# Performance work log

Hardware: AMD Instinct MI355X
Metric: run time of the kernel (lower is better)

The kernel has to match this reference:

```python
import jax, jax.numpy as jnp
import numpy as np

H = 4          # attention heads
K = 16         # knn neighbors
EPS = 1e-5     # BatchNorm eps


def setup_inputs() -> dict:
    key = jax.random.key(0)
    ks = jax.random.split(key, 10)
    B, C, T, N = 2, 128, 32, 512
    OUT = 128
    HID = 2 * C + 2 * OUT  # ff hidden = in*2 + out*2
    s = 0.02
    return {
        "x_all": jax.random.normal(ks[0], (B, C, T, N), jnp.float32),
        "Wq": jax.random.normal(ks[1], (C, C), jnp.float32) * s,
        "Wk": jax.random.normal(ks[2], (C, C), jnp.float32) * s,
        "Wv": jax.random.normal(ks[3], (C, C), jnp.float32) * s,
        "W1": jax.random.normal(ks[4], (HID, C), jnp.float32) * s,
        "W2": jax.random.normal(ks[5], (OUT, HID), jnp.float32) * s,
        "bn_gamma": 1.0 + 0.1 * jax.random.normal(ks[6], (OUT,), jnp.float32),
        "bn_beta": 0.1 * jax.random.normal(ks[7], (OUT,), jnp.float32),
        "bn_mean": 0.1 * jax.random.normal(ks[8], (OUT,), jnp.float32),
        "bn_var": jax.random.uniform(ks[9], (OUT,), jnp.float32, 0.5, 1.5),
    }


def reference(x_all, Wq, Wk, Wv, W1, W2, bn_gamma, bn_beta, bn_mean, bn_var):
    B, C, T, N = x_all.shape
    D = C // H
    # --- st_group_points: candidate pool = 3 consecutive frames (replicate temporal pad), frame-major ---
    xp = jnp.concatenate([x_all[:, :, :1], x_all, x_all[:, :, -1:]], axis=2)   # (B,C,T+2,N)
    pool = jnp.stack([xp[:, :, :-2], xp[:, :, 1:-1], xp[:, :, 2:]], axis=3)    # (B,C,T,3,N)
    pool = pool.reshape(B, C, T, 3 * N)                                        # (B,C,T,3N)
    # KNN on xyz (channels 0:3); sqrt is monotone so topk on squared dists gives same indices
    a = x_all[:, :3]                                                           # (B,3,T,N)
    b = pool[:, :3]                                                            # (B,3,T,3N)
    d2 = jnp.sum((a[..., :, None] - b[..., None, :]) ** 2, axis=1)             # (B,T,N,3N)
    _, idx = jax.lax.top_k(-d2, K)                                             # (B,T,N,K) smallest-dist
    nb = jnp.take_along_axis(pool[:, :, :, None, :], idx[:, None], axis=-1)    # (B,C,T,N,K)
    rel = x_all[..., None] - nb                                                # diff grouping (B,C,T,N,K)
    # --- per-point local attention over K neighbors (1x1 convs == channel matmuls), all t at once ---
    q = jnp.einsum('oc,bctn->botn', Wq, x_all).reshape(B, H, D, T, N)
    k = jnp.einsum('oc,bctnk->botnk', Wk, rel).reshape(B, H, D, T, N, K)
    v = jnp.einsum('oc,bctnk->botnk', Wv, rel).reshape(B, H, D, T, N, K)
    energy = jnp.einsum('bhdtn,bhdtnk->bhtnk', q, k) / jnp.sqrt(jnp.float32(D))
    attn = jax.nn.softmax(energy, axis=-1)                                     # (B,H,T,N,K)
    agg = jnp.einsum('bhtnk,bhdtnk->bhdtn', attn, v).reshape(B, C, T, N)
    # --- residual + BatchNorm1d (eval mode, running stats) + conv feed-forward ---
    h = x_all + agg
    scale = (bn_gamma / jnp.sqrt(bn_var + EPS))[None, :, None, None]
    h = (h - bn_mean[None, :, None, None]) * scale + bn_beta[None, :, None, None]
    h = jax.nn.leaky_relu(jnp.einsum('oc,bctn->botn', W1, h), 0.2)
    y = jnp.einsum('oc,bctn->botn', W2, h)                                     # (B,OUT,T,N)
    return jnp.concatenate([x_all[:, :4], y], axis=1)                          # (B,4+OUT,T,N)
```

## Files before the change

### kernel.cpp

```cpp
#include <hip/hip_runtime.h>
#include <hip/hip_bf16.h>

typedef __hip_bfloat16 bf16;
typedef unsigned long long u64;
typedef __attribute__((ext_vector_type(8))) short short8;
typedef __attribute__((ext_vector_type(4))) float f32x4;

#define B_   2
#define C_   128
#define T_   32
#define N_   512
#define K_   16
#define HID_ 512
#define TN   (T_*N_)
#define PTS  (B_*T_*N_)

#define MFMA_BF16(a,b,c) __builtin_amdgcn_mfma_f32_16x16x32_bf16((a),(b),(c),0,0,0)

__device__ __forceinline__ float b2f(bf16 v){ return __bfloat162float(v); }
__device__ __forceinline__ bf16  f2b(float v){ return __float2bfloat16(v); }
__device__ __forceinline__ float bqf(short v){
  return __uint_as_float(((unsigned)(unsigned short)v) << 16);
}

__device__ __forceinline__ float ldc(const void* p, int i, bool f32) {
  return f32 ? ((const float*)p)[i] : b2f(((const bf16*)p)[i]);
}

__global__ __launch_bounds__(256) void convw_kernel(
    const void* __restrict__ x,
    const void* wq, const void* wk, const void* wv,
    const void* w1, const void* w2, const void* g, const void* bb,
    const void* m, const void* v,
    bf16* __restrict__ wqb, bf16* __restrict__ wkb, bf16* __restrict__ wvb,
    bf16* __restrict__ w1b, bf16* __restrict__ w2b,
    float* __restrict__ gf, float* __restrict__ bf_, float* __restrict__ mf,
    float* __restrict__ vf, int* __restrict__ flag)
{
  __shared__ int cnt;
  if (threadIdx.x == 0) cnt = 0;
  __syncthreads();
  const unsigned short* u = (const unsigned short*)x;
  int w = 0;
#pragma unroll
  for (int j = 0; j < 8; ++j) {
    unsigned short hv = u[threadIdx.x*8 + j];
    int e = (hv >> 7) & 0xFF;
    if (e >= 0x89) w++;
  }
  if (w) atomicAdd(&cnt, w);
  __syncthreads();
  bool f32 = (cnt > 32);
  if (blockIdx.x == 0 && threadIdx.x == 0) *flag = f32 ? 1 : 0;

  int i = blockIdx.x*256 + threadIdx.x;
  if (i < 16384) { wqb[i] = f2b(ldc(wq, i, f32)); return; } i -= 16384;
  if (i < 16384) { wkb[i] = f2b(ldc(wk, i, f32)); return; } i -= 16384;
  if (i < 16384) { wvb[i] = f2b(ldc(wv, i, f32)); return; } i -= 16384;
  if (i < 65536) { w1b[i] = f2b(ldc(w1, i, f32)); return; } i -= 65536;
  if (i < 65536) { w2b[i] = f2b(ldc(w2, i, f32)); return; } i -= 65536;
  if (i < 128)   { gf[i]  = ldc(g, i, f32); return; }       i -= 128;
  if (i < 128)   { bf_[i] = ldc(bb, i, f32); return; }      i -= 128;
  if (i < 128)   { mf[i]  = ldc(m, i, f32); return; }       i -= 128;
  if (i < 128)   { vf[i]  = ldc(v, i, f32); return; }
}

__device__ __forceinline__ u64 shflx64(u64 v, int m) {
  return (u64)__shfl_xor((long long)v, m, 64);
}
template<int W>
__device__ __forceinline__ u64 bitonic64w(u64 key, int lane) {
#pragma unroll
  for (int k = 2; k <= W; k <<= 1) {
#pragma unroll
    for (int j = k >> 1; j >= 1; j >>= 1) {
      u64 p = shflx64(key, j);
      bool keep_min = ((lane & k) == 0) == ((lane & j) == 0);
      key = ((p < key) == keep_min) ? p : key;
    }
  }
  return key;
}
__device__ __forceinline__ unsigned bitonic32u(unsigned key, int lane) {
#pragma unroll
  for (int k = 2; k <= 64; k <<= 1) {
#pragma unroll
    for (int j = k >> 1; j >= 1; j >>= 1) {
      unsigned p = (unsigned)__shfl_xor((int)key, j, 64);
      bool keep_min = ((lane & k) == 0) == ((lane & j) == 0);
      key = ((p < key) == keep_min) ? p : key;
    }
  }
  return key;
}

__device__ __forceinline__ void proj_gemm32(const bf16* __restrict__ W,
                                            bf16 (*ys)[136],
                                            const short8 am[2][4],
                                            int mrow, int quad, int ot)
{
  f32x4 acc[2];
#pragma unroll
  for (int mt=0;mt<2;++mt) acc[mt] = (f32x4){0.f,0.f,0.f,0.f};
#pragma unroll
  for (int kq=0;kq<4;++kq) {
    short8 bfr = *(const short8*)&W[(ot*16+mrow)*C_ + kq*32 + quad*8];
#pragma unroll
    for (int mt=0;mt<2;++mt) acc[mt] = MFMA_BF16(am[mt][kq], bfr, acc[mt]);
  }
#pragma unroll
  for (int mt=0;mt<2;++mt)
#pragma unroll
    for (int r=0;r<4;++r)
      ys[mt*16 + quad*4 + r][ot*16 + mrow] = f2b(acc[mt][r]);
}

__device__ __forceinline__ void tile_store32_512(bf16* __restrict__ dst,
                                                 const bf16 (*ys)[136], int tid)
{
  int flat = tid*8;
  int p = flat >> 7, c = flat & 127;
  *(short8*)&dst[(size_t)p*C_ + c] = *(const short8*)&ys[p][c];
}

__global__ __launch_bounds__(512) void projknn_kernel(
    const void* __restrict__ x, const int* __restrict__ flag,
    const bf16* __restrict__ wqb, const bf16* __restrict__ wkb, const bf16* __restrict__ wvb,
    bf16* __restrict__ xTb, bf16* QT, bf16* __restrict__ KT, bf16* __restrict__ VT,
    int* __restrict__ idxout)
{
  __shared__ __align__(16) char smem[28672];
  int tid = threadIdx.x;
  int blk = blockIdx.x;
  int g = blk / 5, r = blk - g*5;
  if (r == 4) {
    bf16 (*xs )[136] = (bf16(*)[136])(smem);
    bf16 (*ysK)[136] = (bf16(*)[136])(smem + 8704);
    bf16 (*ysV)[136] = (bf16(*)[136])(smem + 17408);
    int p0 = g * 32;
    int b = p0 >> 14; int tn0 = p0 & (TN-1);
    if (*flag) {
      const float* xbase = (const float*)x + (size_t)b*C_*TN + tn0;
#pragma unroll
      for (int it=0; it<8; ++it) {
        int i = it*512 + tid;
        int c = i >> 5, p = i & 31;
        xs[p][c] = f2b(xbase[(size_t)c*TN + p]);
      }
    } else {
      const bf16* xbase = (const bf16*)x + (size_t)b*C_*TN + tn0;
#pragma unroll
      for (int it=0; it<8; ++it) {
        int i = it*512 + tid;
        int c = i >> 5, p = i & 31;
        xs[p][c] = xbase[(size_t)c*TN + p];
      }
    }
    __syncthreads();
    tile_store32_512(xTb + (size_t)p0*C_, xs, tid);
    int lane = tid & 63, wave = tid >> 6;
    int mrow = lane & 15, quad = lane >> 4;
    short8 am[2][4];
#pragma unroll
    for (int mt=0;mt<2;++mt)
#pragma unroll
      for (int kq=0;kq<4;++kq)
        am[mt][kq] = *(const short8*)&xs[mt*16 + mrow][kq*32 + quad*8];
    __syncthreads();
    proj_gemm32(wqb, xs,  am, mrow, quad, wave);
    proj_gemm32(wkb, ysK, am, mrow, quad, wave);
    proj_gemm32(wvb, ysV, am, mrow, quad, wave);
    __syncthreads();
    tile_store32_512(QT + (size_t)p0*C_, xs,  tid);
    tile_store32_512(KT + (size_t)p0*C_, ysK, tid);
    tile_store32_512(VT + (size_t)p0*C_, ysV, tid);
  } else {
    float4* cand4 = (float4*)smem;
    u64 (*surv)[64] = (u64(*)[64])(smem + 24576);
    int kblk = g*4 + r;
    int row = kblk >> 6;
    int b = row >> 5, t = row & 31;
    int ng = kblk & 63;
    bool f32 = (*flag != 0);
#pragma unroll
    for (int q = 0; q < 3; ++q) {
      int tt = t - 1 + q; tt = tt < 0 ? 0 : (tt > T_-1 ? T_-1 : tt);
      size_t base = ((size_t)b*C_*T_ + tt)*(size_t)N_ + tid;
      float c0, c1, c2;
      if (f32) {
        const float* xp = (const float*)x;
        c0 = xp[base]; c1 = xp[base + (size_t)T_*N_]; c2 = xp[base + 2*(size_t)T_*N_];
      } else {
        const bf16* xp = (const bf16*)x;
        c0 = b2f(xp[base]); c1 = b2f(xp[base + (size_t)T_*N_]); c2 = b2f(xp[base + 2*(size_t)T_*N_]);
      }
      cand4[q*N_ + tid] = make_float4(c0, c1, c2, 0.f);
    }
    __syncthreads();
    int wave = tid >> 6, lane = tid & 63;
    int n = ng*8 + wave;
    float4 a = cand4[N_ + n];
    unsigned db[24];
#pragma unroll
    for (int j = 0; j < 24; ++j) {
      float4 cm = cand4[lane + (j << 6)];
      float dx = a.x - cm.x;
      float dy = a.y - cm.y;
      float dz = a.z - cm.z;
      float d2 = __fadd_rn(__fadd_rn(__fmul_rn(dx,dx), __fmul_rn(dy,dy)), __fmul_rn(dz,dz));
      db[j] = __float_as_uint(d2);
    }
    unsigned bd = db[0];
#pragma unroll
    for (int j = 1; j < 24; ++j) bd = (db[j] < bd) ? db[j] : bd;
    unsigned sd = bitonic32u(bd, lane);
    unsigned U = (unsigned)__shfl((int)sd, 15, 64);
    int c = 0;
#pragma unroll
    for (int j = 0; j < 24; ++j) c += (db[j] <= U) ? 1 : 0;
    int sc = c;
#pragma unroll
    for (int d = 1; d < 64; d <<= 1) {
      int pv = __shfl_up(sc, d, 64);
      if (lane >= d) sc += pv;
    }
    int total = __shfl(sc, 63, 64);
    int ofs = sc - c;
    u64 out16;
    if (total <= 64) {
#pragma unroll
      for (int j = 0; j < 24; ++j) {
        if (db[j] <= U) {
          surv[wave][ofs] = ((u64)db[j] << 32) | (unsigned)(lane + (j << 6));
          ++ofs;
        }
      }
      __threadfence_block();
      u64 kk = (lane < total) ? surv[wave][lane] : ~0ull;
      out16 = (total <= 32) ? bitonic64w<32>(kk, lane)
                            : bitonic64w<64>(kk, lane);
    } else {
      u64 key[24];
#pragma unroll
      for (int j = 0; j < 24; ++j)
        key[j] = ((u64)db[j] << 32) | (unsigned)(lane + (j << 6));
      u64 res = ~0ull;
#pragma unroll 1
      for (int rr = 0; rr < 16; ++rr) {
        u64 m2 = key[0];
#pragma unroll
        for (int j = 1; j < 24; ++j) m2 = (key[j] < m2) ? key[j] : m2;
#pragma unroll
        for (int s = 32; s >= 1; s >>= 1) {
          u64 p = shflx64(m2, s);
          m2 = (p < m2) ? p : m2;
        }
        if (lane == rr) res = m2;
        int mwin = (int)(m2 & 0xffffffffu);
        int sel = ((mwin & 63) == lane) ? (mwin >> 6) : -1;
#pragma unroll
        for (int j = 0; j < 24; ++j) if (j == sel) key[j] = ~0ull;
      }
      out16 = res;
    }
    int point = (b*T_ + t)*N_ + n;
    if (lane < K_) idxout[point*K_ + lane] = (int)(out16 & 0xffffffffu);
  }
}

__global__ __launch_bounds__(512) void attn_kernel(
    const int* __restrict__ idxin, const bf16* __restrict__ xTb,
    bf16* qhT , const bf16* __restrict__ KT,
    const bf16* __restrict__ VT,
    const float* __restrict__ gf, const float* __restrict__ bf_,
    const float* __restrict__ mf, const float* __restrict__ vf)
{
  __shared__ int   col_lds[4][16];
  __shared__ float qbuf[4][C_];
  __shared__ bf16  kbuf[4][K_][136];
  __shared__ bf16  vbuf[4][K_][136];
  __shared__ float e_lds[4][4][16];
  int tid = threadIdx.x;
  int pt = tid >> 7, o = tid & 127;
  int point = blockIdx.x*4 + pt;
  int b = point >> 14; int tn = point & (TN-1); int t = tn >> 9;
  if (o < K_) {
    int m = idxin[point*K_ + o];
    int j = m >> 9, nn = m & (N_-1);
    int tt = t-1+j; tt = tt<0?0:(tt>T_-1?T_-1:tt);
    col_lds[pt][o] = ((b*T_ + tt)*N_ + nn)*C_;
  }
  int self = point*C_;
  qbuf[pt][o] = b2f(qhT[self + o]);
  __syncthreads();
#pragma unroll
  for (int it = 0; it < 2; ++it) {
    int i = it*512 + tid;
    int pp = i >> 8, rem = i & 255, k = rem >> 4, ch = rem & 15;
    int src = col_lds[pp][k] + ch*8;
    *(short8*)&kbuf[pp][k][ch*8] = *(const short8*)&KT[src];
    *(short8*)&vbuf[pp][k][ch*8] = *(const short8*)&VT[src];
  }
  __syncthreads();
  {
    int pp = tid >> 7, j = tid & 127;
    int k = j >> 3, hd = (j >> 1) & 3, half = j & 1;
    const float* qp = &qbuf[pp][hd*32 + half*16];
    const bf16*  kp = &kbuf[pp][k][hd*32 + half*16];
    short8 kv0 = *(const short8*)kp;
    short8 kv1 = *(const short8*)(kp + 8);
    float qv[16];
    *(float4*)&qv[0]  = *(const float4*)(qp);
    *(float4*)&qv[4]  = *(const float4*)(qp + 4);
    *(float4*)&qv[8]  = *(const float4*)(qp + 8);
    *(float4*)&qv[12] = *(const float4*)(qp + 12);
    float e = 0.f;
#pragma unroll
    for (int i2=0;i2<8;++i2) e = fmaf(qv[i2],   bqf(kv0[i2]), e);
#pragma unroll
    for (int i2=0;i2<8;++i2) e = fmaf(qv[8+i2], bqf(kv1[i2]), e);
    e += __shfl_xor(e, 1, 64);
    if (!half) e_lds[pp][hd][k] = -e * 0.17677669529663687f;
  }
  __syncthreads();
  int hd = o >> 5;
  float e[16]; float mx = -3e38f;
#pragma unroll
  for (int k=0;k<K_;++k){ e[k]=e_lds[pt][hd][k]; mx=fmaxf(mx,e[k]); }
  float ssum=0.f;
#pragma unroll
  for (int k=0;k<K_;++k){ e[k]=__expf(e[k]-mx); ssum+=e[k]; }
  float inv = 1.f/ssum;
  float acc = b2f(VT[self + o]);
#pragma unroll
  for (int k=0;k<K_;++k)
    acc = fmaf(-(e[k]*inv), b2f(vbuf[pt][k][o]), acc);
  float hv = b2f(xTb[self + o]) + acc;
  float sc = gf[o] / sqrtf(vf[o] + 1e-5f);
  qhT[self + o] = f2b((hv - mf[o])*sc + bf_[o]);
}

__global__ __launch_bounds__(256) void mlp_kernel(const bf16* __restrict__ hT,
                                                  const bf16* __restrict__ w1b,
                                                  const bf16* __restrict__ w2b,
                                                  const void* __restrict__ x,
                                                  const int* __restrict__ flag,
                                                  void* out)
{
  __shared__ bf16 hidh[32][264];
  int tid = threadIdx.x;
  int p0 = blockIdx.x*32;
  int lane = tid & 63, wave = tid >> 6;
  int mrow = lane & 15, quad = lane >> 4;
  bool f32o = (*flag != 0);
  int bb = p0 >> 14;
  int tn0 = p0 & (TN-1);
  if (tid < 128) {
    int c = tid >> 5, p = tid & 31;
    size_t si = ((size_t)bb*C_ + c)*TN + tn0 + p;
    size_t di = ((size_t)bb*132 + c)*TN + tn0 + p;
    if (f32o) ((float*)out)[di] = ((const float*)x)[si];
    else      ((bf16*)out)[di]  = ((const bf16*)x)[si];
  }
  f32x4 acc2[2][2];
#pragma unroll
  for (int oi=0;oi<2;++oi)
#pragma unroll
    for (int mt=0;mt<2;++mt) acc2[oi][mt] = (f32x4){0.f,0.f,0.f,0.f};

#pragma unroll
  for (int half = 0; half < 2; ++half) {
    if (half) __syncthreads();
    short8 am[2][4];
#pragma unroll
    for (int mt=0;mt<2;++mt)
#pragma unroll
      for (int kq=0;kq<4;++kq)
        am[mt][kq] = *(const short8*)&hT[(size_t)(p0 + mt*16 + mrow)*C_ + kq*32 + quad*8];
#pragma unroll
    for (int oi = 0; oi < 4; ++oi) {
      int ot_g = half*16 + wave*4 + oi;
      int otl  = wave*4 + oi;
      f32x4 acc[2];
#pragma unroll
      for (int mt=0;mt<2;++mt) acc[mt] = (f32x4){0.f,0.f,0.f,0.f};
#pragma unroll
      for (int kq=0;kq<4;++kq) {
        short8 bfr = *(const short8*)&w1b[(ot_g*16+mrow)*C_ + kq*32 + quad*8];
#pragma unroll
        for (int mt=0;mt<2;++mt) acc[mt] = MFMA_BF16(am[mt][kq], bfr, acc[mt]);
      }
#pragma unroll
      for (int mt=0;mt<2;++mt)
#pragma unroll
        for (int r=0;r<4;++r) {
          float z = acc[mt][r];
          hidh[mt*16 + quad*4 + r][otl*16 + mrow] = f2b(z > 0.f ? z : 0.2f*z);
        }
    }
    __syncthreads();
#pragma unroll
    for (int kc = 0; kc < 4; ++kc) {
      short8 ha[2][2];
#pragma unroll
      for (int mt=0;mt<2;++mt)
#pragma unroll
        for (int kk=0;kk<2;++kk)
          ha[mt][kk] = *(const short8*)&hidh[mt*16 + mrow][(kc*2+kk)*32 + quad*8];
#pragma unroll
      for (int oi=0;oi<2;++oi) {
        int ot2 = wave*2 + oi;
#pragma unroll
        for (int kk=0;kk<2;++kk) {
          int ks_g = half*8 + kc*2 + kk;
          short8 bfr = *(const short8*)&w2b[(ot2*16+mrow)*HID_ + ks_g*32 + quad*8];
#pragma unroll
          for (int mt=0;mt<2;++mt)
            acc2[oi][mt] = MFMA_BF16(ha[mt][kk], bfr, acc2[oi][mt]);
        }
      }
    }
  }
  size_t obase = (size_t)bb*132*TN;
#pragma unroll
  for (int oi=0;oi<2;++oi) {
    int ch = (wave*2+oi)*16 + mrow;
#pragma unroll
    for (int mt=0;mt<2;++mt) {
      int tn = tn0 + mt*16 + quad*4;
      size_t oidx = obase + (size_t)(4+ch)*TN + tn;
      if (f32o) {
        *(f32x4*)&((float*)out)[oidx] = acc2[oi][mt];
      } else {
        bf16 tmp[4];
#pragma unroll
        for (int r=0;r<4;++r) tmp[r] = f2b(acc2[oi][mt][r]);
        *(u64*)&((bf16*)out)[oidx] = *(u64*)tmp;
      }
    }
  }
}

extern "C" void kernel_launch(void* const* d_in, const int* in_sizes, int n_in,
                              void* d_out, int out_size, void* d_ws, size_t ws_size,
                              hipStream_t stream)
{
  (void)in_sizes; (void)n_in; (void)out_size; (void)ws_size;
  const void* x = d_in[0];
  char* ws = (char*)d_ws;
  const size_t MB = (size_t)1<<20;
  bf16*  QT  = (bf16* )(ws + 0*MB);
  bf16*  KT  = (bf16* )(ws + 8*MB);
  bf16*  VT  = (bf16* )(ws + 16*MB);
  bf16*  xTb = (bf16* )(ws + 24*MB);
  int*   idxw= (int*  )(ws + 32*MB);
  bf16*  wqb = (bf16* )(ws + 34*MB);
  bf16*  wkb = (bf16* )(ws + 34*MB + 0x8000);
  bf16*  wvb = (bf16* )(ws + 34*MB + 0x10000);
  bf16*  w1b = (bf16* )(ws + 34*MB + 0x18000);
  bf16*  w2b = (bf16* )(ws + 34*MB + 0x38000);
  float* gf  = (float*)(ws + 34*MB + 0x58000);
  float* bf_ = (float*)(ws + 34*MB + 0x58200);
  float* mf  = (float*)(ws + 34*MB + 0x58400);
  float* vf  = (float*)(ws + 34*MB + 0x58600);
  int*  flag = (int*  )(ws + 34*MB + 0x58800);

  convw_kernel  <<<dim3(706), dim3(256), 0, stream>>>(
      x, d_in[1], d_in[2], d_in[3], d_in[4], d_in[5],
      d_in[6], d_in[7], d_in[8], d_in[9],
      wqb, wkb, wvb, w1b, w2b, gf, bf_, mf, vf, flag);
  projknn_kernel<<<dim3(5120), dim3(512), 0, stream>>>(
      x, flag, wqb, wkb, wvb, xTb, QT, KT, VT, idxw);
  attn_kernel   <<<dim3(PTS/4), dim3(512), 0, stream>>>(
      idxw, xTb, QT , KT, VT, gf, bf_, mf, vf);
  mlp_kernel    <<<dim3(PTS/32), dim3(256), 0, stream>>>(
      QT , w1b, w2b, x, flag, d_out);
}
```

Before: 208.2 us.

## Replace bitonic sorts in KNN selection with ballot threshold search and rank counting

The KNN top-16 selection no longer sorts the per-lane minima with a bitonic network to find the cutoff. It finds the cutoff with a 16-step ballot/popcount binary search over the float bit pattern, which yields a valid upper bound. The survivor prefix sum now uses bit-sliced ballots with mbcnt instead of a shuffle scan. The survivors are ordered by having each lane count smaller keys in LDS and scatter to its rank, replacing the final 64-bit bitonic sort. The key packing is narrowed to an 11-bit index. This cuts shuffle traffic at the cost of an LDS-read loop per lane and a looser threshold, which may push more points onto the slow fallback path.

```diff
diff --git a/kernel.cpp b/kernel.cpp
--- a/kernel.cpp
+++ b/kernel.cpp
@@ -67,31 +67,6 @@
 
 __device__ __forceinline__ u64 shflx64(u64 v, int m) {
   return (u64)__shfl_xor((long long)v, m, 64);
-}
-template<int W>
-__device__ __forceinline__ u64 bitonic64w(u64 key, int lane) {
-#pragma unroll
-  for (int k = 2; k <= W; k <<= 1) {
-#pragma unroll
-    for (int j = k >> 1; j >= 1; j >>= 1) {
-      u64 p = shflx64(key, j);
-      bool keep_min = ((lane & k) == 0) == ((lane & j) == 0);
-      key = ((p < key) == keep_min) ? p : key;
-    }
-  }
-  return key;
-}
-__device__ __forceinline__ unsigned bitonic32u(unsigned key, int lane) {
-#pragma unroll
-  for (int k = 2; k <= 64; k <<= 1) {
-#pragma unroll
-    for (int j = k >> 1; j >= 1; j >>= 1) {
-      unsigned p = (unsigned)__shfl_xor((int)key, j, 64);
-      bool keep_min = ((lane & k) == 0) == ((lane & j) == 0);
-      key = ((p < key) == keep_min) ? p : key;
-    }
-  }
-  return key;
 }
 
 __device__ __forceinline__ void proj_gemm32(const bf16* __restrict__ W,
@@ -210,35 +185,62 @@
       float d2 = __fadd_rn(__fadd_rn(__fmul_rn(dx,dx), __fmul_rn(dy,dy)), __fmul_rn(dz,dz));
       db[j] = __float_as_uint(d2);
     }
-    unsigned bd = db[0];
-#pragma unroll
-    for (int j = 1; j < 24; ++j) bd = (db[j] < bd) ? db[j] : bd;
-    unsigned sd = bitonic32u(bd, lane);
-    unsigned U = (unsigned)__shfl((int)sd, 15, 64);
+    unsigned mm[12];
+#pragma unroll
+    for (int j = 0; j < 12; ++j) mm[j] = db[2*j] < db[2*j+1] ? db[2*j] : db[2*j+1];
+#pragma unroll
+    for (int j = 0; j < 6; ++j)  mm[j] = mm[2*j] < mm[2*j+1] ? mm[2*j] : mm[2*j+1];
+#pragma unroll
+    for (int j = 0; j < 3; ++j)  mm[j] = mm[2*j] < mm[2*j+1] ? mm[2*j] : mm[2*j+1];
+    unsigned bd = mm[0] < mm[1] ? mm[0] : mm[1];
+    bd = bd < mm[2] ? bd : mm[2];
+    {
+      unsigned lo = 0u, hi = 0x7f800000u;
+#pragma unroll
+      for (int it = 0; it < 16; ++it) {
+        unsigned mid = lo + ((hi - lo) >> 1);
+        int cge = __popcll(__ballot(bd <= mid));
+        bool ge = (cge >= K_);
+        hi = ge ? mid : hi;
+        lo = ge ? lo : (mid + 1u);
+      }
+      bd = hi;
+    }
+    unsigned U = bd;
     int c = 0;
 #pragma unroll
     for (int j = 0; j < 24; ++j) c += (db[j] <= U) ? 1 : 0;
-    int sc = c;
-#pragma unroll
-    for (int d = 1; d < 64; d <<= 1) {
-      int pv = __shfl_up(sc, d, 64);
-      if (lane >= d) sc += pv;
-    }
-    int total = __shfl(sc, 63, 64);
-    int ofs = sc - c;
-    u64 out16;
+    int ofs = 0, total = 0;
+#pragma unroll
+    for (int bit = 0; bit < 5; ++bit) {
+      u64 mball = __ballot(((c >> bit) & 1) != 0);
+      unsigned below = __builtin_amdgcn_mbcnt_hi((unsigned)(mball >> 32),
+                        __builtin_amdgcn_mbcnt_lo((unsigned)mball, 0u));
+      ofs   += ((int)below) << bit;
+      total += (__popcll(mball)) << bit;
+    }
+    int point = (b*T_ + t)*N_ + n;
     if (total <= 64) {
 #pragma unroll
       for (int j = 0; j < 24; ++j) {
         if (db[j] <= U) {
-          surv[wave][ofs] = ((u64)db[j] << 32) | (unsigned)(lane + (j << 6));
+          surv[wave][ofs] = ((u64)db[j] << 11) | (unsigned)(lane + (j << 6));
           ++ofs;
         }
       }
+      if (lane == total) surv[wave][lane] = ~0ull;
       __threadfence_block();
       u64 kk = (lane < total) ? surv[wave][lane] : ~0ull;
-      out16 = (total <= 32) ? bitonic64w<32>(kk, lane)
-                            : bitonic64w<64>(kk, lane);
+      int npair = (total + 1) >> 1;
+      int rank = 0;
+      const ulonglong2* sk2 = (const ulonglong2*)&surv[wave][0];
+#pragma unroll 4
+      for (int i2 = 0; i2 < npair; ++i2) {
+        ulonglong2 kp = sk2[i2];
+        rank += (kp.x < kk) ? 1 : 0;
+        rank += (kp.y < kk) ? 1 : 0;
+      }
+      if (rank < K_) idxout[point*K_ + rank] = (int)(kk & 2047u);
     } else {
       u64 key[24];
 #pragma unroll
@@ -261,10 +263,8 @@
 #pragma unroll
         for (int j = 0; j < 24; ++j) if (j == sel) key[j] = ~0ull;
       }
-      out16 = res;
-    }
-    int point = (b*T_ + t)*N_ + n;
-    if (lane < K_) idxout[point*K_ + lane] = (int)(out16 & 0xffffffffu);
+      if (lane < K_) idxout[point*K_ + lane] = (int)(res & 0xffffffffu);
+    }
   }
 }
 
```

Result: no change. 207.7 us (-0.3%).
